# Optimization experiments

Measured on AMD Instinct MI355X. Metric: run time of the kernel, lower is better.

The kernel has to match this reference:

```python
import jax, jax.numpy as jnp
import numpy as np
from functools import partial

N_QUBITS = 8
DEPTH = 2
INPUT_DIM = 128
HIDDEN_DIM = N_QUBITS  # required: hx = o * tanh(cx) elementwise
DIM = 2 ** N_QUBITS

# Z expectation matrix: ZMAT[k, i] = +1/-1 depending on bit of basis state k at wire i
# (wire 0 is the most-significant qubit, PennyLane convention)
_bits = ((np.arange(DIM)[:, None] >> (N_QUBITS - 1 - np.arange(N_QUBITS)[None, :])) & 1)
ZMAT = jnp.asarray(1.0 - 2.0 * _bits, dtype=jnp.float32)  # [2**n, n]


def _apply_1q(state, G, wire):
    """Apply 2x2 gate G ([2,2] shared or [B,2,2] batched) on `wire`."""
    B = state.shape[0]
    left, right = 2 ** wire, 2 ** (N_QUBITS - wire - 1)
    s = state.reshape(B, left, 2, right)
    if G.ndim == 2:
        s = jnp.einsum('ij,bljr->blir', G, s)
    else:
        s = jnp.einsum('bij,bljr->blir', G, s)
    return s.reshape(B, DIM)


def _apply_cnot(state, wire):
    """CNOT with control=wire, target=wire+1 (adjacent)."""
    B = state.shape[0]
    left, right = 2 ** wire, 2 ** (N_QUBITS - wire - 2)
    s = state.reshape(B, left, 2, 2, right)
    s = jnp.concatenate([s[:, :, :1], s[:, :, 1:, ::-1]], axis=2)
    return s.reshape(B, DIM)


def quantum_gate(angles, params):
    """angles: [B, n] RX rotation angles; params: [depth, n] RY angles.
    Returns [B, n] PauliZ expectations (exact statevector simulation)."""
    B = angles.shape[0]
    state = jnp.zeros((B, DIM), dtype=jnp.complex64).at[:, 0].set(1.0)
    # RX encoding layer (batched angles)
    c = jnp.cos(angles / 2).astype(jnp.complex64)
    s = (-1j) * jnp.sin(angles / 2).astype(jnp.complex64)
    for i in range(N_QUBITS):
        G = jnp.stack([jnp.stack([c[:, i], s[:, i]], -1),
                       jnp.stack([s[:, i], c[:, i]], -1)], -2)  # [B,2,2]
        state = _apply_1q(state, G, i)
    # variational layers: RY (shared params) + CNOT chain
    cp = jnp.cos(params / 2).astype(jnp.complex64)
    sp = jnp.sin(params / 2).astype(jnp.complex64)
    for d in range(DEPTH):
        for i in range(N_QUBITS):
            G = jnp.array([[1.0, 0.0], [0.0, 1.0]], jnp.complex64)
            G = jnp.stack([jnp.stack([cp[d, i], -sp[d, i]]),
                           jnp.stack([sp[d, i], cp[d, i]])])  # [2,2]
            state = _apply_1q(state, G, i)
        for i in range(N_QUBITS - 1):
            state = _apply_cnot(state, i)
    probs = (state.real ** 2 + state.imag ** 2)  # [B, 2**n]
    return probs @ ZMAT  # [B, n]


def setup_inputs() -> dict:
    key = jax.random.key(0)
    ks = jax.random.split(key, 13)
    T, B = 256, 1024
    cat = INPUT_DIM + HIDDEN_DIM
    lin_scale = 1.0 / np.sqrt(cat)
    d = {'inputs': jax.random.normal(ks[0], (T, B, INPUT_DIM), jnp.float32)}
    for idx, g in enumerate(['f', 'i', 'g', 'o']):
        d[f'W{g}'] = jax.random.uniform(ks[1 + 3 * idx], (N_QUBITS, cat), jnp.float32, -lin_scale, lin_scale)
        d[f'b{g}'] = jax.random.uniform(ks[2 + 3 * idx], (N_QUBITS,), jnp.float32, -lin_scale, lin_scale)
        d[f'P{g}'] = jax.random.normal(ks[3 + 3 * idx], (DEPTH, N_QUBITS), jnp.float32)
    return d


def reference(inputs, Wf, bf, Pf, Wi, bi, Pi, Wg, bg, Pg, Wo, bo, Po):
    T, B, _ = inputs.shape
    h0 = jnp.zeros((B, HIDDEN_DIM), inputs.dtype)
    c0 = jnp.zeros((B, HIDDEN_DIM), inputs.dtype)

    def step(carry, x):
        hx, cx = carry
        comb = jnp.concatenate([x, hx], axis=1)  # [B, input+hidden]
        f = jax.nn.sigmoid(quantum_gate(comb @ Wf.T + bf, Pf))
        i = jax.nn.sigmoid(quantum_gate(comb @ Wi.T + bi, Pi))
        g = jnp.tanh(quantum_gate(comb @ Wg.T + bg, Pg))
        o = jax.nn.sigmoid(quantum_gate(comb @ Wo.T + bo, Po))
        cx = f * cx + i * g
        hx = o * jnp.tanh(cx)
        return (hx, cx), hx

    (hx, cx), outputs = jax.lax.scan(step, (h0, c0), inputs)
    return outputs, (hx, cx)
```

## Files before the change

kernel.cpp:

```cpp
#include <hip/hip_runtime.h>
#include <math.h>

#define TS 256
#define BB 1024
#define NQ 8
#define INDIM 128
#define CATDIM 136
#define INV2PI 0.15915494309189535f
#define LOG2E  1.4426950408889634f

typedef float v2f __attribute__((ext_vector_type(2)));

__device__ __forceinline__ float dpp_xor1(float v) {
    return __int_as_float(__builtin_amdgcn_mov_dpp(__float_as_int(v), 0xB1, 0xF, 0xF, true));
}
__device__ __forceinline__ float dpp_xor2(float v) {
    return __int_as_float(__builtin_amdgcn_mov_dpp(__float_as_int(v), 0x4E, 0xF, 0xF, true));
}
__device__ __forceinline__ float dpp_xor8(float v) {
    return __int_as_float(__builtin_amdgcn_mov_dpp(__float_as_int(v), 0x128, 0xF, 0xF, true));
}
__device__ __forceinline__ float swz4(float v)  {
    return __int_as_float(__builtin_amdgcn_ds_swizzle(__float_as_int(v), 0x101F));
}
__device__ __forceinline__ float swz16(float v) {
    return __int_as_float(__builtin_amdgcn_ds_swizzle(__float_as_int(v), 0x401F));
}
__device__ __forceinline__ float swz20(float v) {
    return __int_as_float(__builtin_amdgcn_ds_swizzle(__float_as_int(v), 0x501F));
}
__device__ __forceinline__ float hw_sin(float x) { float r; asm("v_sin_f32 %0, %1" : "=v"(r) : "v"(x)); return r; }
__device__ __forceinline__ float hw_cos(float x) { float r; asm("v_cos_f32 %0, %1" : "=v"(r) : "v"(x)); return r; }
__device__ __forceinline__ float hw_exp(float x) { float r; asm("v_exp_f32 %0, %1" : "=v"(r) : "v"(x)); return r; }
__device__ __forceinline__ float hw_rcp(float x) { float r; asm("v_rcp_f32 %0, %1" : "=v"(r) : "v"(x)); return r; }
__device__ __forceinline__ v2f mk2(float x, float y) { v2f r; r.x = x; r.y = y; return r; }
__device__ __forceinline__ v2f pk_mul(v2f a, v2f b) {
    v2f d; asm("v_pk_mul_f32 %0, %1, %2" : "=v"(d) : "v"(a), "v"(b)); return d;
}
__device__ __forceinline__ v2f pk_fma(v2f a, v2f b, v2f c) {
    v2f d; asm("v_pk_fma_f32 %0, %1, %2, %3" : "=v"(d) : "v"(a), "v"(b), "v"(c)); return d;
}

__launch_bounds__(256)
__global__ void qlstm_xproj(const float* __restrict__ x,
    const float* __restrict__ Wf, const float* __restrict__ bf,
    const float* __restrict__ Wi, const float* __restrict__ bi,
    const float* __restrict__ Wg, const float* __restrict__ bg,
    const float* __restrict__ Wo, const float* __restrict__ bo,
    float* __restrict__ xproj)
{
    const int b = blockIdx.x;
    const int wv = threadIdx.x >> 6;
    const int lane = threadIdx.x & 63;
    const int q = lane >> 3;
    const int kg = lane & 7;

    const float* Ws[4] = { Wf, Wi, Wg, Wo };
    const float* bs[4] = { bf, bi, bg, bo };
    float4 wfrag[4][4];
    float bias_w[4];
    #pragma unroll
    for (int g = 0; g < 4; ++g) {
        const float* Wq = Ws[g] + q * CATDIM + kg * 16;
        #pragma unroll
        for (int c4 = 0; c4 < 4; ++c4) {
            float4 v = *(const float4*)(Wq + c4 * 4);
            v.x *= INV2PI; v.y *= INV2PI; v.z *= INV2PI; v.w *= INV2PI;
            wfrag[g][c4] = v;
        }
        bias_w[g] = bs[g][q] * INV2PI;
    }

    float4 xv[4];
    {
        const float* xr = x + ((size_t)wv * BB + b) * INDIM + kg * 16;
        #pragma unroll
        for (int c4 = 0; c4 < 4; ++c4) xv[c4] = *(const float4*)(xr + c4 * 4);
    }

    #pragma unroll 2
    for (int i = 0; i < 64; ++i) {
        const int t = wv + i * 4;
        float4 xn[4];
        {
            int t2 = (i < 63) ? t + 4 : t;
            const float* xr = x + ((size_t)t2 * BB + b) * INDIM + kg * 16;
            #pragma unroll
            for (int c4 = 0; c4 < 4; ++c4) xn[c4] = *(const float4*)(xr + c4 * 4);
        }
        float* outrow = xproj + ((size_t)b * TS + t) * 32;
        #pragma unroll
        for (int g = 0; g < 4; ++g) {
            float p =
                xv[0].x*wfrag[g][0].x + xv[0].y*wfrag[g][0].y + xv[0].z*wfrag[g][0].z + xv[0].w*wfrag[g][0].w +
                xv[1].x*wfrag[g][1].x + xv[1].y*wfrag[g][1].y + xv[1].z*wfrag[g][1].z + xv[1].w*wfrag[g][1].w +
                xv[2].x*wfrag[g][2].x + xv[2].y*wfrag[g][2].y + xv[2].z*wfrag[g][2].z + xv[2].w*wfrag[g][2].w +
                xv[3].x*wfrag[g][3].x + xv[3].y*wfrag[g][3].y + xv[3].z*wfrag[g][3].z + xv[3].w*wfrag[g][3].w;
            p += dpp_xor1(p);
            p += dpp_xor2(p);
            p += __shfl_xor(p, 4, 64);
            if (kg == 0) outrow[g * 8 + q] = p + bias_w[g];
        }
        xv[0] = xn[0]; xv[1] = xn[1]; xv[2] = xn[2]; xv[3] = xn[3];
    }
}

__launch_bounds__(64, 1)
__global__ void qlstm_v(const float* __restrict__ xproj,
    const float* __restrict__ Wf, const float* __restrict__ Pf,
    const float* __restrict__ Wi, const float* __restrict__ Pi,
    const float* __restrict__ Wg, const float* __restrict__ Pg,
    const float* __restrict__ Wo, const float* __restrict__ Po,
    float* __restrict__ out, float* __restrict__ hst, float* __restrict__ cst)
{
    const int lane = threadIdx.x;
    const int q = (lane & 1) | (lane & 2) | ((lane >> 1) & 4);
    const int g = ((lane >> 2) & 1) | ((lane >> 3) & 2);
    const int el2 = lane >> 5;
    const int b = blockIdx.x * 2 + el2;

    const float* W; const float* P;
    if (g == 0)      { W = Wf; P = Pf; }
    else if (g == 1) { W = Wi; P = Pi; }
    else if (g == 2) { W = Wg; P = Pg; }
    else             { W = Wo; P = Po; }

    float Chw[8], nSw[8], hsp0[8], cp0c[8];
    #pragma unroll
    for (int w = 0; w < 8; ++w) {
        float s1, c1, s0, c0;
        __sincosf(P[8 + w], &s1, &c1);
        __sincosf(P[w], &s0, &c0);
        Chw[w] = 0.5f * c1;
        nSw[w] = -s1;
        hsp0[w] = 0.5f * s0;
        cp0c[w] = c0;
    }

    v2f whp[8][4];
    #pragma unroll
    for (int j = 0; j < 8; ++j) {
        const float* Wj = W + j * CATDIM + INDIM;
        #pragma unroll
        for (int p2 = 0; p2 < 4; ++p2)
            whp[j][p2] = mk2(INV2PI * Wj[q ^ (2 * p2)], INV2PI * Wj[q ^ (2 * p2 + 1)]);
    }

    const float kk = (g == 2) ? 2.f : -1.f;
    const float kl = kk * LOG2E;
    const float Aa = (g == 2) ? 1.f : 0.f;
    const float Bb = (g == 2) ? -1.f : 1.f;
    float sel[8];
    #pragma unroll
    for (int i = 0; i < 8; ++i) sel[i] = (q == i) ? kl : 0.f;

    float s0h = 0.f, s1h = 0.f, s2h = 0.f, s3h = 0.f;
    float s4h = 0.f, s5h = 0.f, s6h = 0.f, s7h = 0.f;
    float c_own = 0.f, hv = 0.f;

    const float* xbase = xproj + ((size_t)b * TS) * 32 + g * 8;
    float4 xv0 = *(const float4*)(xbase);
    float4 xv1 = *(const float4*)(xbase + 4);

    for (int t = 0; t < TS; ++t) {
        v2f hp0 = mk2(s0h, s1h), hp1 = mk2(s2h, s3h);
        v2f hp2 = mk2(s4h, s5h), hp3 = mk2(s6h, s7h);
        float xq[8] = { xv0.x, xv0.y, xv0.z, xv0.w, xv1.x, xv1.y, xv1.z, xv1.w };
        float sa[8], ca[8];
        #pragma unroll
        for (int j = 0; j < 8; ++j) {
            v2f acc = pk_fma(hp0, whp[j][0], mk2(xq[j], 0.f));
            acc = pk_fma(hp1, whp[j][1], acc);
            acc = pk_fma(hp2, whp[j][2], acc);
            acc = pk_fma(hp3, whp[j][3], acc);
            float ang = acc.x + acc.y;
            sa[j] = hw_sin(ang);
            ca[j] = hw_cos(ang);
        }

        {
            int tn = (t + 1 < TS) ? t + 1 : t;
            xv0 = *(const float4*)(xbase + (size_t)tn * 32);
            xv1 = *(const float4*)(xbase + (size_t)tn * 32 + 4);
        }

        float kE = 0.f;
        float d0, d1, zr, zi;
        {
            float AmB = cp0c[0] * ca[0];
            float gr = hsp0[0] * ca[0];
            float gi = -0.5f * sa[0];
            d0 = Chw[0] * (1.f + AmB);
            d1 = -(Chw[0] * (1.f - AmB));
            zr = nSw[0] * gr;
            zi = nSw[0] * gi;
        }
        #pragma unroll
        for (int w = 1; w < 8; ++w) {
            float gr = hsp0[w] * ca[w];
            float gi = -0.5f * sa[w];
            float AmB = cp0c[w] * ca[w];
            float sum = d0 + d1, dif = d0 - d1;
            float p = gr * zr, qv = gi * zi;
            float Ew = fmaf(4.f, p, sum);
            kE = fmaf(sel[w - 1], Ew, kE);
            float ad = AmB * dif;
            float e1 = sum + ad, e3 = sum - ad;
            float e2 = p - qv, e4 = p + qv;
            float T0 = fmaf(4.f, e2, e1);
            float T1 = fmaf(4.f, e4, e3);
            float f1 = fmaf(gr, sum, zr);
            float f2 = gi * dif;
            float f3 = fmaf(AmB, zi, f2);
            d0 = Chw[w] * T0;
            d1 = -(Chw[w] * T1);
            zr = nSw[w] * f1;
            zi = nSw[w] * f3;
        }
        {
            float E7 = (d0 + d1) + 2.f * zr;
            kE = fmaf(sel[7], E7, kE);
        }

        float y = hw_exp(kE);
        float a = fmaf(Aa, y, Bb) * hw_rcp(y + 1.f);

        float b4 = swz4(a);
        float b16 = swz16(a);
        float b20 = swz20(a);
        bool g1b = (g & 2) != 0;
        bool g0b = (g & 1) != 0;
        float e0 = g1b ? b16 : a;
        float e1s = g1b ? b20 : b4;
        float e2s = g1b ? a : b16;
        float e3s = g1b ? b4 : b20;
        float fv = g0b ? e1s : e0;
        float iv = g0b ? e0 : e1s;
        float gv = g0b ? e3s : e2s;
        float ov = g0b ? e2s : e3s;

        c_own = fmaf(fv, c_own, iv * gv);
        float e2c = hw_exp(c_own * (2.f * LOG2E));
        hv = ov * ((e2c - 1.f) * hw_rcp(e2c + 1.f));

        if ((lane & 0x14) == 0)
            out[((size_t)t * BB + b) * NQ + q] = hv;

        s0h = hv;
        s1h = dpp_xor1(s0h);
        s2h = dpp_xor2(s0h);
        s3h = dpp_xor2(s1h);
        s4h = dpp_xor8(s0h);
        s5h = dpp_xor8(s1h);
        s6h = dpp_xor8(s2h);
        s7h = dpp_xor8(s3h);
    }

    if ((lane & 0x14) == 0) {
        hst[b * NQ + q] = hv;
        cst[b * NQ + q] = c_own;
    }
}

extern "C" void kernel_launch(void* const* d_in, const int* in_sizes, int n_in,
                              void* d_out, int out_size, void* d_ws, size_t ws_size,
                              hipStream_t stream) {
    const float* x  = (const float*)d_in[0];
    const float* Wf = (const float*)d_in[1];
    const float* bf = (const float*)d_in[2];
    const float* Pf = (const float*)d_in[3];
    const float* Wi = (const float*)d_in[4];
    const float* bi = (const float*)d_in[5];
    const float* Pi = (const float*)d_in[6];
    const float* Wg = (const float*)d_in[7];
    const float* bg = (const float*)d_in[8];
    const float* Pg = (const float*)d_in[9];
    const float* Wo = (const float*)d_in[10];
    const float* bo = (const float*)d_in[11];
    const float* Po = (const float*)d_in[12];

    float* out = (float*)d_out;
    float* hst = out + (size_t)TS * BB * NQ;
    float* cst = hst + (size_t)BB * NQ;
    float* xproj = (float*)d_ws;

    qlstm_xproj<<<BB, 256, 0, stream>>>(x, Wf, bf, Wi, bi, Wg, bg, Wo, bo, xproj);
    qlstm_v<<<BB / 2, 64, 0, stream>>>(xproj, Wf, Pf, Wi, Pi, Wg, Pg, Wo, Po,
                                       out, hst, cst);
}
```

Measured before the change: 238.3 us.

## Fuse input projection into recurrent kernel with cross-lane reduction and bpermute broadcast

Drops the separate xproj kernel and its workspace round-trip. The recurrent kernel now computes the x·W projection itself: each lane handles 16 input columns for 8 rows, then a DPP transpose-reduce gives each lane its own qubit's angle. Each lane then computes sin/cos for only its own angle, and the eight values the state simulation needs are gathered with ds_bpermute. The cost is more per-step ALU work and LDS-permute latency on the serial recurrence critical path, in exchange for removing a kernel launch and the global-memory intermediate.

```diff
diff --git a/kernel.cpp b/kernel.cpp
--- a/kernel.cpp
+++ b/kernel.cpp
@@ -29,6 +29,9 @@
 __device__ __forceinline__ float swz20(float v) {
     return __int_as_float(__builtin_amdgcn_ds_swizzle(__float_as_int(v), 0x501F));
 }
+__device__ __forceinline__ float bperm(int addr, float v) {
+    return __int_as_float(__builtin_amdgcn_ds_bpermute(addr, __float_as_int(v)));
+}
 __device__ __forceinline__ float hw_sin(float x) { float r; asm("v_sin_f32 %0, %1" : "=v"(r) : "v"(x)); return r; }
 __device__ __forceinline__ float hw_cos(float x) { float r; asm("v_cos_f32 %0, %1" : "=v"(r) : "v"(x)); return r; }
 __device__ __forceinline__ float hw_exp(float x) { float r; asm("v_exp_f32 %0, %1" : "=v"(r) : "v"(x)); return r; }
@@ -41,89 +44,26 @@
     v2f d; asm("v_pk_fma_f32 %0, %1, %2, %3" : "=v"(d) : "v"(a), "v"(b), "v"(c)); return d;
 }
 
-__launch_bounds__(256)
-__global__ void qlstm_xproj(const float* __restrict__ x,
-    const float* __restrict__ Wf, const float* __restrict__ bf,
-    const float* __restrict__ Wi, const float* __restrict__ bi,
-    const float* __restrict__ Wg, const float* __restrict__ bg,
-    const float* __restrict__ Wo, const float* __restrict__ bo,
-    float* __restrict__ xproj)
-{
-    const int b = blockIdx.x;
-    const int wv = threadIdx.x >> 6;
-    const int lane = threadIdx.x & 63;
-    const int q = lane >> 3;
-    const int kg = lane & 7;
-
-    const float* Ws[4] = { Wf, Wi, Wg, Wo };
-    const float* bs[4] = { bf, bi, bg, bo };
-    float4 wfrag[4][4];
-    float bias_w[4];
-    #pragma unroll
-    for (int g = 0; g < 4; ++g) {
-        const float* Wq = Ws[g] + q * CATDIM + kg * 16;
-        #pragma unroll
-        for (int c4 = 0; c4 < 4; ++c4) {
-            float4 v = *(const float4*)(Wq + c4 * 4);
-            v.x *= INV2PI; v.y *= INV2PI; v.z *= INV2PI; v.w *= INV2PI;
-            wfrag[g][c4] = v;
-        }
-        bias_w[g] = bs[g][q] * INV2PI;
-    }
-
-    float4 xv[4];
-    {
-        const float* xr = x + ((size_t)wv * BB + b) * INDIM + kg * 16;
-        #pragma unroll
-        for (int c4 = 0; c4 < 4; ++c4) xv[c4] = *(const float4*)(xr + c4 * 4);
-    }
-
-    #pragma unroll 2
-    for (int i = 0; i < 64; ++i) {
-        const int t = wv + i * 4;
-        float4 xn[4];
-        {
-            int t2 = (i < 63) ? t + 4 : t;
-            const float* xr = x + ((size_t)t2 * BB + b) * INDIM + kg * 16;
-            #pragma unroll
-            for (int c4 = 0; c4 < 4; ++c4) xn[c4] = *(const float4*)(xr + c4 * 4);
-        }
-        float* outrow = xproj + ((size_t)b * TS + t) * 32;
-        #pragma unroll
-        for (int g = 0; g < 4; ++g) {
-            float p =
-                xv[0].x*wfrag[g][0].x + xv[0].y*wfrag[g][0].y + xv[0].z*wfrag[g][0].z + xv[0].w*wfrag[g][0].w +
-                xv[1].x*wfrag[g][1].x + xv[1].y*wfrag[g][1].y + xv[1].z*wfrag[g][1].z + xv[1].w*wfrag[g][1].w +
-                xv[2].x*wfrag[g][2].x + xv[2].y*wfrag[g][2].y + xv[2].z*wfrag[g][2].z + xv[2].w*wfrag[g][2].w +
-                xv[3].x*wfrag[g][3].x + xv[3].y*wfrag[g][3].y + xv[3].z*wfrag[g][3].z + xv[3].w*wfrag[g][3].w;
-            p += dpp_xor1(p);
-            p += dpp_xor2(p);
-            p += __shfl_xor(p, 4, 64);
-            if (kg == 0) outrow[g * 8 + q] = p + bias_w[g];
-        }
-        xv[0] = xn[0]; xv[1] = xn[1]; xv[2] = xn[2]; xv[3] = xn[3];
-    }
-}
-
 __launch_bounds__(64, 1)
-__global__ void qlstm_v(const float* __restrict__ xproj,
-    const float* __restrict__ Wf, const float* __restrict__ Pf,
-    const float* __restrict__ Wi, const float* __restrict__ Pi,
-    const float* __restrict__ Wg, const float* __restrict__ Pg,
-    const float* __restrict__ Wo, const float* __restrict__ Po,
+__global__ void qlstm_f(const float* __restrict__ x,
+    const float* __restrict__ Wf, const float* __restrict__ bf, const float* __restrict__ Pf,
+    const float* __restrict__ Wi, const float* __restrict__ bi, const float* __restrict__ Pi,
+    const float* __restrict__ Wg, const float* __restrict__ bg, const float* __restrict__ Pg,
+    const float* __restrict__ Wo, const float* __restrict__ bo, const float* __restrict__ Po,
     float* __restrict__ out, float* __restrict__ hst, float* __restrict__ cst)
 {
     const int lane = threadIdx.x;
-    const int q = (lane & 1) | (lane & 2) | ((lane >> 1) & 4);
+    const int l0 = lane & 1, l1 = (lane >> 1) & 1, l3 = (lane >> 3) & 1;
+    const int q = 4 * l0 + 2 * l1 + l3;
     const int g = ((lane >> 2) & 1) | ((lane >> 3) & 2);
     const int el2 = lane >> 5;
     const int b = blockIdx.x * 2 + el2;
 
-    const float* W; const float* P;
-    if (g == 0)      { W = Wf; P = Pf; }
-    else if (g == 1) { W = Wi; P = Pi; }
-    else if (g == 2) { W = Wg; P = Pg; }
-    else             { W = Wo; P = Po; }
+    const float* W; const float* P; const float* bs;
+    if (g == 0)      { W = Wf; P = Pf; bs = bf; }
+    else if (g == 1) { W = Wi; P = Pi; bs = bi; }
+    else if (g == 2) { W = Wg; P = Pg; bs = bg; }
+    else             { W = Wo; P = Po; bs = bo; }
 
     float Chw[8], nSw[8], hsp0[8], cp0c[8];
     #pragma unroll
@@ -137,17 +77,36 @@
         cp0c[w] = c0;
     }
 
-    v2f whp[8][4];
+    v2f xw[8][8];
     #pragma unroll
     for (int j = 0; j < 8; ++j) {
-        const float* Wj = W + j * CATDIM + INDIM;
+        const float* Wj = W + j * CATDIM + 16 * q;
+        #pragma unroll
+        for (int p2 = 0; p2 < 4; ++p2) {
+            float4 v = *(const float4*)(Wj + p2 * 4);
+            xw[j][p2*2]   = mk2(INV2PI * v.x, INV2PI * v.y);
+            xw[j][p2*2+1] = mk2(INV2PI * v.z, INV2PI * v.w);
+        }
+    }
+
+    v2f whq[4];
+    {
+        const float* Wq = W + q * CATDIM + INDIM;
         #pragma unroll
         for (int p2 = 0; p2 < 4; ++p2)
-            whp[j][p2] = mk2(INV2PI * Wj[q ^ (2 * p2)], INV2PI * Wj[q ^ (2 * p2 + 1)]);
-    }
-
-    const float kk = (g == 2) ? 2.f : -1.f;
-    const float kl = kk * LOG2E;
+            whq[p2] = mk2(INV2PI * Wq[q ^ (2 * p2)], INV2PI * Wq[q ^ (2 * p2 + 1)]);
+    }
+    const float bq = INV2PI * bs[q];
+
+    int badr[8];
+    {
+        int base = lane & 0x34;
+        #pragma unroll
+        for (int w = 0; w < 8; ++w)
+            badr[w] = (base | ((w >> 2) & 1) | (((w >> 1) & 1) << 1) | ((w & 1) << 3)) << 2;
+    }
+
+    const float kl = ((g == 2) ? 2.f : -1.f) * LOG2E;
     const float Aa = (g == 2) ? 1.f : 0.f;
     const float Bb = (g == 2) ? -1.f : 1.f;
     float sel[8];
@@ -158,48 +117,82 @@
     float s4h = 0.f, s5h = 0.f, s6h = 0.f, s7h = 0.f;
     float c_own = 0.f, hv = 0.f;
 
-    const float* xbase = xproj + ((size_t)b * TS) * 32 + g * 8;
-    float4 xv0 = *(const float4*)(xbase);
-    float4 xv1 = *(const float4*)(xbase + 4);
+    const float* xptr = x + (size_t)b * INDIM + 16 * q;
+    float4 xv0 = *(const float4*)(xptr);
+    float4 xv1 = *(const float4*)(xptr + 4);
+    float4 xv2 = *(const float4*)(xptr + 8);
+    float4 xv3 = *(const float4*)(xptr + 12);
+    xptr += (size_t)BB * INDIM;
 
     for (int t = 0; t < TS; ++t) {
-        v2f hp0 = mk2(s0h, s1h), hp1 = mk2(s2h, s3h);
-        v2f hp2 = mk2(s4h, s5h), hp3 = mk2(s6h, s7h);
-        float xq[8] = { xv0.x, xv0.y, xv0.z, xv0.w, xv1.x, xv1.y, xv1.z, xv1.w };
-        float sa[8], ca[8];
+        v2f xc[8] = { mk2(xv0.x, xv0.y), mk2(xv0.z, xv0.w),
+                      mk2(xv1.x, xv1.y), mk2(xv1.z, xv1.w),
+                      mk2(xv2.x, xv2.y), mk2(xv2.z, xv2.w),
+                      mk2(xv3.x, xv3.y), mk2(xv3.z, xv3.w) };
+        float pt[8];
         #pragma unroll
         for (int j = 0; j < 8; ++j) {
-            v2f acc = pk_fma(hp0, whp[j][0], mk2(xq[j], 0.f));
-            acc = pk_fma(hp1, whp[j][1], acc);
-            acc = pk_fma(hp2, whp[j][2], acc);
-            acc = pk_fma(hp3, whp[j][3], acc);
-            float ang = acc.x + acc.y;
-            sa[j] = hw_sin(ang);
-            ca[j] = hw_cos(ang);
-        }
-
-        {
-            int tn = (t + 1 < TS) ? t + 1 : t;
-            xv0 = *(const float4*)(xbase + (size_t)tn * 32);
-            xv1 = *(const float4*)(xbase + (size_t)tn * 32 + 4);
+            v2f acc = pk_mul(xc[0], xw[j][0]);
+            acc = pk_fma(xc[1], xw[j][1], acc);
+            acc = pk_fma(xc[2], xw[j][2], acc);
+            acc = pk_fma(xc[3], xw[j][3], acc);
+            acc = pk_fma(xc[4], xw[j][4], acc);
+            acc = pk_fma(xc[5], xw[j][5], acc);
+            acc = pk_fma(xc[6], xw[j][6], acc);
+            acc = pk_fma(xc[7], xw[j][7], acc);
+            pt[j] = acc.x + acc.y;
+        }
+
+        {
+            float4 xn0 = *(const float4*)(xptr);
+            float4 xn1 = *(const float4*)(xptr + 4);
+            float4 xn2 = *(const float4*)(xptr + 8);
+            float4 xn3 = *(const float4*)(xptr + 12);
+            xptr += (t < TS - 2) ? (size_t)BB * INDIM : 0;
+            xv0 = xn0; xv1 = xn1; xv2 = xn2; xv3 = xn3;
+        }
+
+        {
+            float s, r;
+            s = l0 ? pt[0] : pt[4]; r = dpp_xor1(s); pt[0] = (l0 ? pt[4] : pt[0]) + r;
+            s = l0 ? pt[1] : pt[5]; r = dpp_xor1(s); pt[1] = (l0 ? pt[5] : pt[1]) + r;
+            s = l0 ? pt[2] : pt[6]; r = dpp_xor1(s); pt[2] = (l0 ? pt[6] : pt[2]) + r;
+            s = l0 ? pt[3] : pt[7]; r = dpp_xor1(s); pt[3] = (l0 ? pt[7] : pt[3]) + r;
+            s = l1 ? pt[0] : pt[2]; r = dpp_xor2(s); pt[0] = (l1 ? pt[2] : pt[0]) + r;
+            s = l1 ? pt[1] : pt[3]; r = dpp_xor2(s); pt[1] = (l1 ? pt[3] : pt[1]) + r;
+            s = l3 ? pt[0] : pt[1]; r = dpp_xor8(s); pt[0] = (l3 ? pt[1] : pt[0]) + r;
+        }
+
+        v2f hacc = pk_fma(mk2(s0h, s1h), whq[0], mk2(pt[0] + bq, 0.f));
+        hacc = pk_fma(mk2(s2h, s3h), whq[1], hacc);
+        hacc = pk_fma(mk2(s4h, s5h), whq[2], hacc);
+        hacc = pk_fma(mk2(s6h, s7h), whq[3], hacc);
+        float ang = hacc.x + hacc.y;
+
+        float sa_own = hw_sin(ang);
+        float ca_own = hw_cos(ang);
+
+        float saw[8], caw[8];
+        #pragma unroll
+        for (int w = 0; w < 8; ++w) {
+            saw[w] = bperm(badr[w], sa_own);
+            caw[w] = bperm(badr[w], ca_own);
         }
 
         float kE = 0.f;
         float d0, d1, zr, zi;
         {
-            float AmB = cp0c[0] * ca[0];
-            float gr = hsp0[0] * ca[0];
-            float gi = -0.5f * sa[0];
+            float AmB = cp0c[0] * caw[0];
             d0 = Chw[0] * (1.f + AmB);
             d1 = -(Chw[0] * (1.f - AmB));
-            zr = nSw[0] * gr;
-            zi = nSw[0] * gi;
+            zr = nSw[0] * (hsp0[0] * caw[0]);
+            zi = nSw[0] * (-0.5f * saw[0]);
         }
         #pragma unroll
         for (int w = 1; w < 8; ++w) {
-            float gr = hsp0[w] * ca[w];
-            float gi = -0.5f * sa[w];
-            float AmB = cp0c[w] * ca[w];
+            float gr = hsp0[w] * caw[w];
+            float gi = -0.5f * saw[w];
+            float AmB = cp0c[w] * caw[w];
             float sum = d0 + d1, dif = d0 - d1;
             float p = gr * zr, qv = gi * zi;
             float Ew = fmaf(4.f, p, sum);
@@ -210,8 +203,7 @@
             float T0 = fmaf(4.f, e2, e1);
             float T1 = fmaf(4.f, e4, e3);
             float f1 = fmaf(gr, sum, zr);
-            float f2 = gi * dif;
-            float f3 = fmaf(AmB, zi, f2);
+            float f3 = fmaf(AmB, zi, gi * dif);
             d0 = Chw[w] * T0;
             d1 = -(Chw[w] * T1);
             zr = nSw[w] * f1;
@@ -247,13 +239,13 @@
             out[((size_t)t * BB + b) * NQ + q] = hv;
 
         s0h = hv;
-        s1h = dpp_xor1(s0h);
+        s4h = dpp_xor1(s0h);
         s2h = dpp_xor2(s0h);
-        s3h = dpp_xor2(s1h);
-        s4h = dpp_xor8(s0h);
-        s5h = dpp_xor8(s1h);
-        s6h = dpp_xor8(s2h);
-        s7h = dpp_xor8(s3h);
+        s6h = dpp_xor2(s4h);
+        s1h = dpp_xor8(s0h);
+        s5h = dpp_xor8(s4h);
+        s3h = dpp_xor8(s2h);
+        s7h = dpp_xor8(s6h);
     }
 
     if ((lane & 0x14) == 0) {
@@ -282,9 +274,8 @@
     float* out = (float*)d_out;
     float* hst = out + (size_t)TS * BB * NQ;
     float* cst = hst + (size_t)BB * NQ;
-    float* xproj = (float*)d_ws;
-
-    qlstm_xproj<<<BB, 256, 0, stream>>>(x, Wf, bf, Wi, bi, Wg, bg, Wo, bo, xproj);
-    qlstm_v<<<BB / 2, 64, 0, stream>>>(xproj, Wf, Pf, Wi, Pi, Wg, Pg, Wo, Po,
+
+    qlstm_f<<<BB / 2, 64, 0, stream>>>(x, Wf, bf, Pf, Wi, bi, Pi,
+                                       Wg, bg, Pg, Wo, bo, Po,
                                        out, hst, cst);
 }
```

Result: no change. 236.4 us (-0.8%).
